# Kernel optimization log

Measured on AMD Instinct MI355X. Metric: run time of the kernel, lower is better.

## Reference

```python
import jax, jax.numpy as jnp
import numpy as np

N_HEAD = 16
L_PARAM = 2  # module's L; min block = 2**L


def _build_sets(T, Lp):
    sets = []
    L = 2 ** Lp
    while L <= T:
        for i in range(T // L):
            sets.append((i * L, (i + 1) * L - 1))
        L *= 2
    return np.asarray(sets, dtype=np.int32)  # [nsets, 2]


def _get_slice(x_cum, l_idx, r_idx):
    # x_cum: [B, nh, T, hs]; returns cumulative-sum slice sums for each (l, r)
    r = x_cum[:, :, r_idx, :]
    l = x_cum[:, :, l_idx - 1, :] * (l_idx >= 1)[None, None, :, None]
    return r - l


def setup_inputs() -> dict:
    key = jax.random.key(0)
    k1, k2, k3 = jax.random.split(key, 3)
    B, T, C = 2, 2048, 1024
    x = jax.random.normal(k1, (B, T, C), dtype=jnp.float32)
    W_attn = jax.random.normal(k2, (3 * C, C), dtype=jnp.float32) * 0.02
    W_proj = jax.random.normal(k3, (C, C), dtype=jnp.float32) * 0.02
    return {"x": x, "W_attn": W_attn, "W_proj": W_proj}


def reference(x, W_attn, W_proj):
    B, T, C = x.shape
    nh, hs = N_HEAD, C // N_HEAD
    scale = 1.0 / np.sqrt(hs).astype(np.float32)

    qkv = x @ W_attn.T  # [B, T, 3C]
    q, k, v = jnp.split(qkv, 3, axis=2)
    q = q.reshape(B, T, nh, hs).transpose(0, 2, 1, 3)  # [B, nh, T, hs]
    k = k.reshape(B, T, nh, hs).transpose(0, 2, 1, 3)
    v = v.reshape(B, T, nh, hs).transpose(0, 2, 1, 3)

    # phi is identity, so q_phi = q, k_phi = k
    k_cum = jnp.cumsum(k, axis=2)
    v_cum = jnp.cumsum(v, axis=2)

    sets = _build_sets(T, L_PARAM)  # static, [nsets, 2]
    l_idx = jnp.asarray(sets[:, 0])
    r_idx = jnp.asarray(sets[:, 1])

    K = _get_slice(k_cum, l_idx, r_idx)  # [B, nh, nsets, hs]
    V = _get_slice(v_cum, l_idx, r_idx)

    t = jnp.arange(T)
    mask = t[:, None] >= r_idx[None, :]  # [T, nsets]

    att_logits = jnp.einsum('bhtd,bhsd->bhts', q, K) * scale
    att_logits = jnp.where(mask[None, None], att_logits, -jnp.inf)

    # tail term: remaining t % 2**L + 1 keys for each query
    Lmin = 2 ** L_PARAM
    tail_len = t % Lmin + 1
    l_tail = t - tail_len + 1
    K_tail = _get_slice(k_cum, l_tail, t)  # [B, nh, T, hs]
    V_tail = _get_slice(v_cum, l_tail, t)
    att_tail = jnp.sum(q * K_tail, axis=-1) * scale  # [B, nh, T]

    logits = jnp.concatenate([att_logits, att_tail[..., None]], axis=-1)
    att = jax.nn.softmax(logits, axis=-1)

    out = jnp.einsum('bhts,bhsd->bhtd', att[..., :-1], V) + att[..., -1:] * V_tail
    out = out.transpose(0, 2, 1, 3).reshape(B, T, C)
    return out @ W_proj.T
```

## Files before the change

kernel.cpp:

```cpp
#include <hip/hip_runtime.h>

typedef _Float16 f16x8 __attribute__((ext_vector_type(8)));
typedef unsigned short u16x8 __attribute__((ext_vector_type(8)));
typedef float f32x4  __attribute__((ext_vector_type(4)));
typedef unsigned short u16;

#define T_SEQ 2048
#define C_DIM 1024
#define NH 16
#define HS 64
#define S_SETS 1023
#define S_PAD 1024
#define SCALE 0.125f
#define NEG_BIG -1e30f

#define GLB(p) ((const __attribute__((address_space(1))) void*)(p))
#define LDS(p) ((__attribute__((address_space(3))) void*)(p))

__device__ __forceinline__ u16 f2h(float f) {
    _Float16 h = (_Float16)f;
    return __builtin_bit_cast(unsigned short, h);
}
__device__ __forceinline__ float h2f(u16 u) {
    _Float16 h = __builtin_bit_cast(_Float16, u);
    return (float)h;
}
__device__ __forceinline__ f32x4 mfmah(f16x8 a, f16x8 b, f32x4 c) {
    return __builtin_amdgcn_mfma_f32_16x16x32_f16(a, b, c, 0, 0, 0);
}

__global__ __launch_bounds__(256) void conv_all(const float* __restrict__ x,
                                                const float* __restrict__ wa,
                                                const float* __restrict__ wp,
                                                u16* __restrict__ x16,
                                                u16* __restrict__ wa16,
                                                u16* __restrict__ wp16) {
    int i = blockIdx.x * 256 + threadIdx.x;
    const float* src; u16* dst; int off;
    if (i < 1048576)              { src = x;  dst = x16;  off = i; }
    else if (i < 1048576 + 786432){ src = wa; dst = wa16; off = i - 1048576; }
    else                          { src = wp; dst = wp16; off = i - (1048576 + 786432); }
    float4 f = ((const float4*)src)[off];
    ushort4 o;
    o.x = f2h(f.x); o.y = f2h(f.y); o.z = f2h(f.z); o.w = f2h(f.w);
    ((ushort4*)dst)[off] = o;
}

__global__ __launch_bounds__(256) void gemm_qkv16(const u16* __restrict__ x16,
                                                  const u16* __restrict__ wa16,
                                                  u16* __restrict__ q16,
                                                  u16* __restrict__ k16,
                                                  u16* __restrict__ v16) {
    __shared__ u16 As[128 * 32];
    __shared__ u16 Bs[128 * 32];
    int tid = threadIdx.x, wv = tid >> 6, lane = tid & 63;
    int lm = lane & 15, quad = lane >> 4;
    int mt = blockIdx.x / 24, nt = blockIdx.x % 24;
    int wm = wv >> 1, wn = wv & 1;
    int m_off = wm * 64, n_off = wn * 64;

    const u16* gsrc;
    u16* ldst;
    int half = wv & 1;
    if (wv < 2) { gsrc = x16  + (size_t)(mt * 128 + half * 64) * C_DIM; ldst = As + half * 64 * 32; }
    else        { gsrc = wa16 + (size_t)(nt * 128 + half * 64) * C_DIM; ldst = Bs + half * 64 * 32; }
    int srow = lane >> 2, scol = (lane & 3) * 8;

    f32x4 acc[4][4];
    #pragma unroll
    for (int i = 0; i < 4; ++i)
        #pragma unroll
        for (int j = 0; j < 4; ++j) acc[i][j] = (f32x4){0.f, 0.f, 0.f, 0.f};

    for (int k0 = 0; k0 < C_DIM; k0 += 32) {
        __syncthreads();
        #pragma unroll
        for (int i = 0; i < 4; ++i) {
            int row = i * 16 + srow;
            __builtin_amdgcn_global_load_lds(
                GLB(gsrc + (size_t)row * C_DIM + k0 + scol),
                LDS(ldst + i * 512), 16, 0, 0);
        }
        __syncthreads();
        f16x8 af[4], bf[4];
        #pragma unroll
        for (int i = 0; i < 4; ++i) {
            af[i] = *(const f16x8*)(As + (m_off + i * 16 + lm) * 32 + quad * 8);
            bf[i] = *(const f16x8*)(Bs + (n_off + i * 16 + lm) * 32 + quad * 8);
        }
        #pragma unroll
        for (int mi = 0; mi < 4; ++mi)
            #pragma unroll
            for (int ni = 0; ni < 4; ++ni)
                acc[mi][ni] = mfmah(af[mi], bf[ni], acc[mi][ni]);
    }

    #pragma unroll
    for (int mi = 0; mi < 4; ++mi)
        #pragma unroll
        for (int ni = 0; ni < 4; ++ni) {
            int n = nt * 128 + n_off + ni * 16 + lm;
            int which = n >> 10, h = (n >> 6) & 15, d = n & 63;
            #pragma unroll
            for (int reg = 0; reg < 4; ++reg) {
                int m = mt * 128 + m_off + mi * 16 + quad * 4 + reg;
                int b_ = m >> 11, t = m & 2047;
                size_t oi = (((size_t)(b_ * NH + h)) * T_SEQ + t) * HS + d;
                float val = acc[mi][ni][reg];
                if (which == 0)      q16[oi] = f2h(val * SCALE);
                else if (which == 1) k16[oi] = f2h(val);
                else                 v16[oi] = f2h(val);
            }
        }
}

__global__ __launch_bounds__(256) void set_sums(const u16* __restrict__ k16,
                                                const u16* __restrict__ v16,
                                                u16* __restrict__ K16,
                                                u16* __restrict__ VT16) {
    int bh  = blockIdx.x;
    int src = blockIdx.y >> 2;
    int dc  = blockIdx.y & 3;
    int tid = threadIdx.x;
    __shared__ float lv0[512 * 16];
    __shared__ float lv1[256 * 16];
    const u16* sp = src ? v16 : k16;
    u16* op = src ? VT16 : K16;
    int dbase = dc * 16;
    if (tid < 16) {
        int d = dbase + tid;
        size_t o = src ? ((size_t)bh * HS + d) * S_PAD + 1023
                       : ((size_t)bh * S_PAD + 1023) * HS + d;
        op[o] = 0;
    }
    for (int idx = tid; idx < 512 * 16; idx += 256) {
        int sg = idx >> 4, dd = idx & 15, d = dbase + dd;
        const u16* p = sp + ((size_t)bh * T_SEQ + sg * 4) * HS + d;
        float s = h2f(p[0]) + h2f(p[HS]) + h2f(p[2 * HS]) + h2f(p[3 * HS]);
        lv0[sg * 16 + dd] = s;
        size_t o = src ? ((size_t)bh * HS + d) * S_PAD + sg
                       : ((size_t)bh * S_PAD + sg) * HS + d;
        op[o] = f2h(s);
    }
    __syncthreads();
    int nsets = 256, offset = 512, lvl = 1;
    while (nsets >= 1) {
        float* sbuf = (lvl & 1) ? lv0 : lv1;
        float* dbuf = (lvl & 1) ? lv1 : lv0;
        for (int idx = tid; idx < nsets * 16; idx += 256) {
            int i = idx >> 4, dd = idx & 15, d = dbase + dd;
            float s = sbuf[(2 * i) * 16 + dd] + sbuf[(2 * i + 1) * 16 + dd];
            dbuf[i * 16 + dd] = s;
            int so = offset + i;
            size_t o = src ? ((size_t)bh * HS + d) * S_PAD + so
                           : ((size_t)bh * S_PAD + so) * HS + d;
            op[o] = f2h(s);
        }
        __syncthreads();
        offset += nsets; nsets >>= 1; lvl++;
    }
}

__global__ __launch_bounds__(256) void attn_flash16(const u16* __restrict__ q16,
                                                    const u16* __restrict__ K16,
                                                    const u16* __restrict__ VT16,
                                                    u16* __restrict__ Opart,
                                                    float* __restrict__ LSEpart) {
    int bh = blockIdx.x;
    int half = blockIdx.z;
    int tid = threadIdx.x, wv = tid >> 6, lane = tid & 63;
    int lm = lane & 15, quad = lane >> 4;
    int tgrp = (wv < 2) ? (32 * blockIdx.y) : (2016 - 32 * blockIdx.y);
    int t0w = tgrp + (wv & 1) * 16;
    int twmax = t0w + 15;
    int sbase = half * 512;

    __shared__ u16 Ks[2][64 * 64];
    __shared__ u16 Pbuf[4][16 * 72];
    __shared__ u16 rtab[512];

    const u16* qg = q16 + ((size_t)bh * T_SEQ + t0w + lm) * HS;
    f16x8 a0 = *(const f16x8*)(qg + quad * 8);
    f16x8 a1 = *(const f16x8*)(qg + 32 + quad * 8);

    #pragma unroll
    for (int i = tid; i < 512; i += 256) {
        int s = sbase + i;
        unsigned rv = 0xFFFFu;
        if (s < S_SETS) {
            int e = S_SETS - s;
            int l = __clz(e) - 22;
            int i0 = s - (1024 - (1024 >> l));
            rv = (unsigned)((i0 + 1) * (4 << l) - 1);
        }
        rtab[i] = (u16)rv;
    }

    f32x4 O[4];
    #pragma unroll
    for (int i = 0; i < 4; ++i) O[i] = (f32x4){0.f, 0.f, 0.f, 0.f};
    f32x4 mrun = (f32x4){NEG_BIG, NEG_BIG, NEG_BIG, NEG_BIG};
    f32x4 lsum = (f32x4){0.f, 0.f, 0.f, 0.f};

    u16* Pw = &Pbuf[wv][0];
    const u16* vb  = VT16 + (size_t)bh * HS * S_PAD;
    const u16* kbh = K16  + ((size_t)bh * S_PAD + sbase) * HS;

    int l8 = lane >> 3;
    int lg = (lane & 7) ^ l8;
    const u16* gsw = kbh + (size_t)(wv * 16 + l8) * HS + lg * 8;

    __builtin_amdgcn_global_load_lds(GLB(gsw),       LDS(&Ks[0][wv * 1024]),       16, 0, 0);
    __builtin_amdgcn_global_load_lds(GLB(gsw + 512), LDS(&Ks[0][wv * 1024 + 512]), 16, 0, 0);
    __syncthreads();

    for (int c = 0; c < 8; ++c) {
        int cur = c & 1;
        int s0 = sbase + c * 64;
        const u16* Ksb = &Ks[cur][0];

        if (c < 7) {
            const u16* gn = gsw + (size_t)(c + 1) * 4096;
            __builtin_amdgcn_global_load_lds(GLB(gn),       LDS(&Ks[cur ^ 1][wv * 1024]),       16, 0, 0);
            __builtin_amdgcn_global_load_lds(GLB(gn + 512), LDS(&Ks[cur ^ 1][wv * 1024 + 512]), 16, 0, 0);
        }

        int r4[4];
        #pragma unroll
        for (int st = 0; st < 4; ++st) r4[st] = rtab[c * 64 + st * 16 + lm];

        unsigned flags = 0;
        f32x4 lt[4];
        #pragma unroll
        for (int st = 0; st < 4; ++st) {
            int r = r4[st];
            unsigned long long bal = __ballot(r <= twmax);
            if (bal) {
                flags |= 1u << st;
                int sl = st * 16 + lm, sx = sl & 7;
                f16x8 b0 = *(const f16x8*)(Ksb + sl * 64 + ((quad ^ sx) << 3));
                f16x8 b1 = *(const f16x8*)(Ksb + sl * 64 + (((4 + quad) ^ sx) << 3));
                f32x4 a = (f32x4){0.f, 0.f, 0.f, 0.f};
                a = mfmah(a0, b0, a);
                a = mfmah(a1, b1, a);
                #pragma unroll
                for (int reg = 0; reg < 4; ++reg) {
                    int t = t0w + quad * 4 + reg;
                    lt[st][reg] = (t >= r) ? a[reg] : NEG_BIG;
                }
            }
        }

        if (flags) {
            bool need = false;
            #pragma unroll
            for (int st = 0; st < 4; ++st)
                if ((flags >> st) & 1u)
                    #pragma unroll
                    for (int reg = 0; reg < 4; ++reg)
                        need |= lt[st][reg] > mrun[reg] + 8.f;
            if (__ballot(need)) {
                f32x4 mc = (f32x4){NEG_BIG, NEG_BIG, NEG_BIG, NEG_BIG};
                #pragma unroll
                for (int st = 0; st < 4; ++st)
                    if ((flags >> st) & 1u)
                        #pragma unroll
                        for (int reg = 0; reg < 4; ++reg)
                            mc[reg] = fmaxf(mc[reg], lt[st][reg]);
                #pragma unroll
                for (int off = 1; off < 16; off <<= 1)
                    #pragma unroll
                    for (int reg = 0; reg < 4; ++reg)
                        mc[reg] = fmaxf(mc[reg], __shfl_xor(mc[reg], off));
                #pragma unroll
                for (int reg = 0; reg < 4; ++reg) {
                    float mnew = fmaxf(mrun[reg], mc[reg]);
                    float alpha = __expf(mrun[reg] - mnew);
                    lsum[reg] *= alpha;
                    #pragma unroll
                    for (int dt = 0; dt < 4; ++dt) O[dt][reg] *= alpha;
                    mrun[reg] = mnew;
                }
            }
            #pragma unroll
            for (int st = 0; st < 4; ++st) {
                if ((flags >> st) & 1u) {
                    #pragma unroll
                    for (int reg = 0; reg < 4; ++reg) {
                        float lv = lt[st][reg];
                        float p = (lv > -5e29f) ? __expf(lv - mrun[reg]) : 0.f;
                        lsum[reg] += p;
                        Pw[(quad * 4 + reg) * 72 + st * 16 + lm] = f2h(p);
                    }
                } else {
                    #pragma unroll
                    for (int reg = 0; reg < 4; ++reg)
                        Pw[(quad * 4 + reg) * 72 + st * 16 + lm] = 0;
                }
            }

            #pragma unroll
            for (int kc = 0; kc < 2; ++kc) {
                if (!((flags >> (2 * kc)) & 3u)) continue;
                f16x8 afr = *(const f16x8*)(Pw + lm * 72 + kc * 32 + quad * 8);
                #pragma unroll
                for (int dt = 0; dt < 4; ++dt) {
                    size_t vo = (size_t)(dt * 16 + lm) * S_PAD + s0 + kc * 32 + quad * 8;
                    f16x8 bv = *(const f16x8*)(vb + vo);
                    O[dt] = mfmah(afr, bv, O[dt]);
                }
            }
        }

        if (c < 7) __syncthreads();
    }

    #pragma unroll
    for (int off = 1; off < 16; off <<= 1)
        #pragma unroll
        for (int reg = 0; reg < 4; ++reg) lsum[reg] += __shfl_xor(lsum[reg], off);

    u16* Ob = Opart + ((size_t)half * 32 + bh) * T_SEQ * HS;
    float* Lb = LSEpart + ((size_t)half * 32 + bh) * T_SEQ;
    #pragma unroll
    for (int reg = 0; reg < 4; ++reg) {
        int t = t0w + quad * 4 + reg;
        float inv = lsum[reg] > 0.f ? 1.f / lsum[reg] : 0.f;
        #pragma unroll
        for (int dt = 0; dt < 4; ++dt)
            Ob[(size_t)t * HS + dt * 16 + lm] = f2h(O[dt][reg] * inv);
        if (lm == 0)
            Lb[t] = lsum[reg] > 0.f ? mrun[reg] + __logf(lsum[reg]) : NEG_BIG;
    }
}

__global__ __launch_bounds__(256) void attn_combine(const u16* __restrict__ q16,
                                                    const u16* __restrict__ k16,
                                                    const u16* __restrict__ v16,
                                                    const u16* __restrict__ Opart,
                                                    const float* __restrict__ LSEpart,
                                                    u16* __restrict__ att16) {
    int bh = blockIdx.y;
    int wv = threadIdx.x >> 6, d = threadIdx.x & 63;
    int t = blockIdx.x * 4 + wv;
    size_t row = (size_t)bh * T_SEQ + t;

    float lse0 = LSEpart[row];
    float lse1 = LSEpart[(size_t)32 * T_SEQ + row];

    int len = (t & 3) + 1;
    const u16* kp = k16 + row * HS + d;
    const u16* vp = v16 + row * HS + d;
    float kt = 0.f, vt = 0.f;
    for (int j = 0; j < len; ++j) { kt += h2f(kp[-j * HS]); vt += h2f(vp[-j * HS]); }
    float tl = h2f(q16[row * HS + d]) * kt;
    #pragma unroll
    for (int off = 1; off < 64; off <<= 1) tl += __shfl_xor(tl, off);

    float mf = fmaxf(fmaxf(lse0, lse1), tl);
    float w0 = __expf(lse0 - mf), w1 = __expf(lse1 - mf), wt = __expf(tl - mf);
    float inv = 1.f / (w0 + w1 + wt);
    float o0 = h2f(Opart[row * HS + d]);
    float o1 = h2f(Opart[(size_t)32 * T_SEQ * HS + row * HS + d]);
    float val = (w0 * o0 + w1 * o1 + wt * vt) * inv;

    int b_ = bh >> 4, h_ = bh & 15;
    att16[((size_t)b_ * T_SEQ + t) * C_DIM + h_ * HS + d] = f2h(val);
}

__global__ __launch_bounds__(256) void gemm_proj16(const u16* __restrict__ a_,
                                                   const u16* __restrict__ w,
                                                   float* __restrict__ out) {
    __shared__ u16 As[128 * 32];
    __shared__ u16 Bs[128 * 32];
    int tid = threadIdx.x, wv = tid >> 6, lane = tid & 63;
    int lm = lane & 15, quad = lane >> 4;
    int mt = blockIdx.x >> 3, nt = blockIdx.x & 7;
    int wm = wv >> 1, wn = wv & 1;
    int m_off = wm * 64, n_off = wn * 64;

    const u16* gsrc;
    u16* ldst;
    int half = wv & 1;
    if (wv < 2) { gsrc = a_ + (size_t)(mt * 128 + half * 64) * C_DIM; ldst = As + half * 64 * 32; }
    else        { gsrc = w  + (size_t)(nt * 128 + half * 64) * C_DIM; ldst = Bs + half * 64 * 32; }
    int srow = lane >> 2, scol = (lane & 3) * 8;

    f32x4 acc[4][4];
    #pragma unroll
    for (int i = 0; i < 4; ++i)
        #pragma unroll
        for (int j = 0; j < 4; ++j) acc[i][j] = (f32x4){0.f, 0.f, 0.f, 0.f};

    for (int k0 = 0; k0 < C_DIM; k0 += 32) {
        __syncthreads();
        #pragma unroll
        for (int i = 0; i < 4; ++i) {
            int row = i * 16 + srow;
            __builtin_amdgcn_global_load_lds(
                GLB(gsrc + (size_t)row * C_DIM + k0 + scol),
                LDS(ldst + i * 512), 16, 0, 0);
        }
        __syncthreads();
        f16x8 af[4], bf[4];
        #pragma unroll
        for (int i = 0; i < 4; ++i) {
            af[i] = *(const f16x8*)(As + (m_off + i * 16 + lm) * 32 + quad * 8);
            bf[i] = *(const f16x8*)(Bs + (n_off + i * 16 + lm) * 32 + quad * 8);
        }
        #pragma unroll
        for (int mi = 0; mi < 4; ++mi)
            #pragma unroll
            for (int ni = 0; ni < 4; ++ni)
                acc[mi][ni] = mfmah(af[mi], bf[ni], acc[mi][ni]);
    }

    #pragma unroll
    for (int mi = 0; mi < 4; ++mi)
        #pragma unroll
        for (int ni = 0; ni < 4; ++ni) {
            int n = nt * 128 + n_off + ni * 16 + lm;
            #pragma unroll
            for (int reg = 0; reg < 4; ++reg) {
                int m = mt * 128 + m_off + mi * 16 + quad * 4 + reg;
                out[(size_t)m * C_DIM + n] = acc[mi][ni][reg];
            }
        }
}

extern "C" void kernel_launch(void* const* d_in, const int* in_sizes, int n_in,
                              void* d_out, int out_size, void* d_ws, size_t ws_size,
                              hipStream_t stream) {
    const float* x     = (const float*)d_in[0];
    const float* Wattn = (const float*)d_in[1];
    const float* Wproj = (const float*)d_in[2];
    float* out = (float*)d_out;
    char* ws = (char*)d_ws;
    u16*  Opart = (u16*)(ws + 0);
    u16*  x16   = (u16*)(ws + 0);
    u16*  wa16  = (u16*)(ws + 8388608);
    u16*  q16   = (u16*)(ws + 16777216);
    u16*  k16   = (u16*)(ws + 25165824);
    u16*  v16   = (u16*)(ws + 33554432);
    u16*  K16   = (u16*)(ws + 41943040);
    u16*  VT16  = (u16*)(ws + 46137344);
    u16*  att16 = (u16*)(ws + 50331648);
    float* LSE  = (float*)(ws + 58720256);
    u16*  wp16  = (u16*)(ws + 59244544);

    hipLaunchKernelGGL(conv_all, dim3(8192), dim3(256), 0, stream,
                       x, Wattn, Wproj, x16, wa16, wp16);
    hipLaunchKernelGGL(gemm_qkv16, dim3(768), dim3(256), 0, stream, x16, wa16, q16, k16, v16);
    hipLaunchKernelGGL(set_sums, dim3(32, 8), dim3(256), 0, stream, k16, v16, K16, VT16);
    hipLaunchKernelGGL(attn_flash16, dim3(32, 32, 2), dim3(256), 0, stream,
                       q16, K16, VT16, Opart, LSE);
    hipLaunchKernelGGL(attn_combine, dim3(512, 32), dim3(256), 0, stream,
                       q16, k16, v16, Opart, LSE, att16);
    hipLaunchKernelGGL(gemm_proj16, dim3(256), dim3(256), 0, stream, att16, wp16, out);
}
```

Before: 224.8 us.

## Double-buffer GEMM LDS tiles and switch softmax to base-2 exponent

Both fp16 GEMMs now prefetch the next K-tile into a second LDS buffer while MFMAs run on the current one, which drops one barrier per iteration and overlaps global-to-LDS loads with compute. The attention softmax now uses base-2 math: log2(e) is folded into the q scale, and raw v_exp_f32/v_log_f32 replace __expf/__logf. A finite running-max sentinel lets the masked-value branch in the probability computation be removed, and zero-fill of P subtiles is limited to tiles whose neighbour is active. This doubles GEMM LDS usage, which may lower occupancy, and relies on exp2 of very negative arguments flushing to zero.

```diff
diff --git a/kernel.cpp b/kernel.cpp
--- a/kernel.cpp
+++ b/kernel.cpp
@@ -11,8 +11,9 @@
 #define HS 64
 #define S_SETS 1023
 #define S_PAD 1024
-#define SCALE 0.125f
+#define SCALE2 0.18033688011112042f
 #define NEG_BIG -1e30f
+#define MSENT  -50000.0f
 
 #define GLB(p) ((const __attribute__((address_space(1))) void*)(p))
 #define LDS(p) ((__attribute__((address_space(3))) void*)(p))
@@ -24,6 +25,12 @@
 __device__ __forceinline__ float h2f(u16 u) {
     _Float16 h = __builtin_bit_cast(_Float16, u);
     return (float)h;
+}
+__device__ __forceinline__ float exp2h(float x) {
+    float r; asm("v_exp_f32 %0, %1" : "=v"(r) : "v"(x)); return r;
+}
+__device__ __forceinline__ float log2h(float x) {
+    float r; asm("v_log_f32 %0, %1" : "=v"(r) : "v"(x)); return r;
 }
 __device__ __forceinline__ f32x4 mfmah(f16x8 a, f16x8 b, f32x4 c) {
     return __builtin_amdgcn_mfma_f32_16x16x32_f16(a, b, c, 0, 0, 0);
@@ -51,8 +58,8 @@
                                                   u16* __restrict__ q16,
                                                   u16* __restrict__ k16,
                                                   u16* __restrict__ v16) {
-    __shared__ u16 As[128 * 32];
-    __shared__ u16 Bs[128 * 32];
+    __shared__ u16 As[2][128 * 32];
+    __shared__ u16 Bs[2][128 * 32];
     int tid = threadIdx.x, wv = tid >> 6, lane = tid & 63;
     int lm = lane & 15, quad = lane >> 4;
     int mt = blockIdx.x / 24, nt = blockIdx.x % 24;
@@ -60,10 +67,12 @@
     int m_off = wm * 64, n_off = wn * 64;
 
     const u16* gsrc;
-    u16* ldst;
+    u16 *ldst0, *ldst1;
     int half = wv & 1;
-    if (wv < 2) { gsrc = x16  + (size_t)(mt * 128 + half * 64) * C_DIM; ldst = As + half * 64 * 32; }
-    else        { gsrc = wa16 + (size_t)(nt * 128 + half * 64) * C_DIM; ldst = Bs + half * 64 * 32; }
+    if (wv < 2) { gsrc = x16  + (size_t)(mt * 128 + half * 64) * C_DIM;
+                  ldst0 = &As[0][half * 2048]; ldst1 = &As[1][half * 2048]; }
+    else        { gsrc = wa16 + (size_t)(nt * 128 + half * 64) * C_DIM;
+                  ldst0 = &Bs[0][half * 2048]; ldst1 = &Bs[1][half * 2048]; }
     int srow = lane >> 2, scol = (lane & 3) * 8;
 
     f32x4 acc[4][4];
@@ -72,27 +81,36 @@
         #pragma unroll
         for (int j = 0; j < 4; ++j) acc[i][j] = (f32x4){0.f, 0.f, 0.f, 0.f};
 
-    for (int k0 = 0; k0 < C_DIM; k0 += 32) {
-        __syncthreads();
+    #pragma unroll
+    for (int i = 0; i < 4; ++i)
+        __builtin_amdgcn_global_load_lds(
+            GLB(gsrc + (size_t)(i * 16 + srow) * C_DIM + scol),
+            LDS(ldst0 + i * 512), 16, 0, 0);
+    __syncthreads();
+
+    for (int k0 = 0, it = 0; k0 < C_DIM; k0 += 32, ++it) {
+        const u16* Ab = (it & 1) ? &As[1][0] : &As[0][0];
+        const u16* Bb = (it & 1) ? &Bs[1][0] : &Bs[0][0];
+        if (k0 + 32 < C_DIM) {
+            u16* nd = (it & 1) ? ldst0 : ldst1;
+            #pragma unroll
+            for (int i = 0; i < 4; ++i)
+                __builtin_amdgcn_global_load_lds(
+                    GLB(gsrc + (size_t)(i * 16 + srow) * C_DIM + k0 + 32 + scol),
+                    LDS(nd + i * 512), 16, 0, 0);
+        }
+        f16x8 af[4], bf[4];
         #pragma unroll
         for (int i = 0; i < 4; ++i) {
-            int row = i * 16 + srow;
-            __builtin_amdgcn_global_load_lds(
-                GLB(gsrc + (size_t)row * C_DIM + k0 + scol),
-                LDS(ldst + i * 512), 16, 0, 0);
-        }
-        __syncthreads();
-        f16x8 af[4], bf[4];
-        #pragma unroll
-        for (int i = 0; i < 4; ++i) {
-            af[i] = *(const f16x8*)(As + (m_off + i * 16 + lm) * 32 + quad * 8);
-            bf[i] = *(const f16x8*)(Bs + (n_off + i * 16 + lm) * 32 + quad * 8);
+            af[i] = *(const f16x8*)(Ab + (m_off + i * 16 + lm) * 32 + quad * 8);
+            bf[i] = *(const f16x8*)(Bb + (n_off + i * 16 + lm) * 32 + quad * 8);
         }
         #pragma unroll
         for (int mi = 0; mi < 4; ++mi)
             #pragma unroll
             for (int ni = 0; ni < 4; ++ni)
                 acc[mi][ni] = mfmah(af[mi], bf[ni], acc[mi][ni]);
+        __syncthreads();
     }
 
     #pragma unroll
@@ -107,7 +125,7 @@
                 int b_ = m >> 11, t = m & 2047;
                 size_t oi = (((size_t)(b_ * NH + h)) * T_SEQ + t) * HS + d;
                 float val = acc[mi][ni][reg];
-                if (which == 0)      q16[oi] = f2h(val * SCALE);
+                if (which == 0)      q16[oi] = f2h(val * SCALE2);
                 else if (which == 1) k16[oi] = f2h(val);
                 else                 v16[oi] = f2h(val);
             }
@@ -199,7 +217,7 @@
     f32x4 O[4];
     #pragma unroll
     for (int i = 0; i < 4; ++i) O[i] = (f32x4){0.f, 0.f, 0.f, 0.f};
-    f32x4 mrun = (f32x4){NEG_BIG, NEG_BIG, NEG_BIG, NEG_BIG};
+    f32x4 mrun = (f32x4){MSENT, MSENT, MSENT, MSENT};
     f32x4 lsum = (f32x4){0.f, 0.f, 0.f, 0.f};
 
     u16* Pw = &Pbuf[wv][0];
@@ -252,21 +270,18 @@
         }
 
         if (flags) {
-            bool need = false;
+            f32x4 mc = (f32x4){NEG_BIG, NEG_BIG, NEG_BIG, NEG_BIG};
             #pragma unroll
             for (int st = 0; st < 4; ++st)
                 if ((flags >> st) & 1u)
                     #pragma unroll
                     for (int reg = 0; reg < 4; ++reg)
-                        need |= lt[st][reg] > mrun[reg] + 8.f;
+                        mc[reg] = fmaxf(mc[reg], lt[st][reg]);
+            bool need = false;
+            #pragma unroll
+            for (int reg = 0; reg < 4; ++reg)
+                need |= mc[reg] > mrun[reg] + 8.f;
             if (__ballot(need)) {
-                f32x4 mc = (f32x4){NEG_BIG, NEG_BIG, NEG_BIG, NEG_BIG};
-                #pragma unroll
-                for (int st = 0; st < 4; ++st)
-                    if ((flags >> st) & 1u)
-                        #pragma unroll
-                        for (int reg = 0; reg < 4; ++reg)
-                            mc[reg] = fmaxf(mc[reg], lt[st][reg]);
                 #pragma unroll
                 for (int off = 1; off < 16; off <<= 1)
                     #pragma unroll
@@ -275,7 +290,7 @@
                 #pragma unroll
                 for (int reg = 0; reg < 4; ++reg) {
                     float mnew = fmaxf(mrun[reg], mc[reg]);
-                    float alpha = __expf(mrun[reg] - mnew);
+                    float alpha = exp2h(mrun[reg] - mnew);
                     lsum[reg] *= alpha;
                     #pragma unroll
                     for (int dt = 0; dt < 4; ++dt) O[dt][reg] *= alpha;
@@ -287,12 +302,11 @@
                 if ((flags >> st) & 1u) {
                     #pragma unroll
                     for (int reg = 0; reg < 4; ++reg) {
-                        float lv = lt[st][reg];
-                        float p = (lv > -5e29f) ? __expf(lv - mrun[reg]) : 0.f;
+                        float p = exp2h(lt[st][reg] - mrun[reg]);
                         lsum[reg] += p;
                         Pw[(quad * 4 + reg) * 72 + st * 16 + lm] = f2h(p);
                     }
-                } else {
+                } else if ((flags >> (st ^ 1)) & 1u) {
                     #pragma unroll
                     for (int reg = 0; reg < 4; ++reg)
                         Pw[(quad * 4 + reg) * 72 + st * 16 + lm] = 0;
@@ -330,7 +344,7 @@
         for (int dt = 0; dt < 4; ++dt)
             Ob[(size_t)t * HS + dt * 16 + lm] = f2h(O[dt][reg] * inv);
         if (lm == 0)
-            Lb[t] = lsum[reg] > 0.f ? mrun[reg] + __logf(lsum[reg]) : NEG_BIG;
+            Lb[t] = lsum[reg] > 0.f ? mrun[reg] + log2h(lsum[reg]) : NEG_BIG;
     }
 }
 
@@ -358,7 +372,7 @@
     for (int off = 1; off < 64; off <<= 1) tl += __shfl_xor(tl, off);
 
     float mf = fmaxf(fmaxf(lse0, lse1), tl);
-    float w0 = __expf(lse0 - mf), w1 = __expf(lse1 - mf), wt = __expf(tl - mf);
+    float w0 = exp2h(lse0 - mf), w1 = exp2h(lse1 - mf), wt = exp2h(tl - mf);
     float inv = 1.f / (w0 + w1 + wt);
     float o0 = h2f(Opart[row * HS + d]);
     float o1 = h2f(Opart[(size_t)32 * T_SEQ * HS + row * HS + d]);
@@ -371,8 +385,8 @@
 __global__ __launch_bounds__(256) void gemm_proj16(const u16* __restrict__ a_,
                                                    const u16* __restrict__ w,
                                                    float* __restrict__ out) {
-    __shared__ u16 As[128 * 32];
-    __shared__ u16 Bs[128 * 32];
+    __shared__ u16 As[2][128 * 32];
+    __shared__ u16 Bs[2][128 * 32];
     int tid = threadIdx.x, wv = tid >> 6, lane = tid & 63;
     int lm = lane & 15, quad = lane >> 4;
     int mt = blockIdx.x >> 3, nt = blockIdx.x & 7;
@@ -380,10 +394,12 @@
     int m_off = wm * 64, n_off = wn * 64;
 
     const u16* gsrc;
-    u16* ldst;
+    u16 *ldst0, *ldst1;
     int half = wv & 1;
-    if (wv < 2) { gsrc = a_ + (size_t)(mt * 128 + half * 64) * C_DIM; ldst = As + half * 64 * 32; }
-    else        { gsrc = w  + (size_t)(nt * 128 + half * 64) * C_DIM; ldst = Bs + half * 64 * 32; }
+    if (wv < 2) { gsrc = a_ + (size_t)(mt * 128 + half * 64) * C_DIM;
+                  ldst0 = &As[0][half * 2048]; ldst1 = &As[1][half * 2048]; }
+    else        { gsrc = w  + (size_t)(nt * 128 + half * 64) * C_DIM;
+                  ldst0 = &Bs[0][half * 2048]; ldst1 = &Bs[1][half * 2048]; }
     int srow = lane >> 2, scol = (lane & 3) * 8;
 
     f32x4 acc[4][4];
@@ -392,27 +408,36 @@
         #pragma unroll
         for (int j = 0; j < 4; ++j) acc[i][j] = (f32x4){0.f, 0.f, 0.f, 0.f};
 
-    for (int k0 = 0; k0 < C_DIM; k0 += 32) {
-        __syncthreads();
+    #pragma unroll
+    for (int i = 0; i < 4; ++i)
+        __builtin_amdgcn_global_load_lds(
+            GLB(gsrc + (size_t)(i * 16 + srow) * C_DIM + scol),
+            LDS(ldst0 + i * 512), 16, 0, 0);
+    __syncthreads();
+
+    for (int k0 = 0, it = 0; k0 < C_DIM; k0 += 32, ++it) {
+        const u16* Ab = (it & 1) ? &As[1][0] : &As[0][0];
+        const u16* Bb = (it & 1) ? &Bs[1][0] : &Bs[0][0];
+        if (k0 + 32 < C_DIM) {
+            u16* nd = (it & 1) ? ldst0 : ldst1;
+            #pragma unroll
+            for (int i = 0; i < 4; ++i)
+                __builtin_amdgcn_global_load_lds(
+                    GLB(gsrc + (size_t)(i * 16 + srow) * C_DIM + k0 + 32 + scol),
+                    LDS(nd + i * 512), 16, 0, 0);
+        }
+        f16x8 af[4], bf[4];
         #pragma unroll
         for (int i = 0; i < 4; ++i) {
-            int row = i * 16 + srow;
-            __builtin_amdgcn_global_load_lds(
-                GLB(gsrc + (size_t)row * C_DIM + k0 + scol),
-                LDS(ldst + i * 512), 16, 0, 0);
-        }
-        __syncthreads();
-        f16x8 af[4], bf[4];
-        #pragma unroll
-        for (int i = 0; i < 4; ++i) {
-            af[i] = *(const f16x8*)(As + (m_off + i * 16 + lm) * 32 + quad * 8);
-            bf[i] = *(const f16x8*)(Bs + (n_off + i * 16 + lm) * 32 + quad * 8);
+            af[i] = *(const f16x8*)(Ab + (m_off + i * 16 + lm) * 32 + quad * 8);
+            bf[i] = *(const f16x8*)(Bb + (n_off + i * 16 + lm) * 32 + quad * 8);
         }
         #pragma unroll
         for (int mi = 0; mi < 4; ++mi)
             #pragma unroll
             for (int ni = 0; ni < 4; ++ni)
                 acc[mi][ni] = mfmah(af[mi], bf[ni], acc[mi][ni]);
+        __syncthreads();
     }
 
     #pragma unroll
```

After: 221.9 us. About the same (-1.3%).
